# Optimization experiments

Hardware: AMD Instinct MI355X
Metric: run time of the kernel (lower is better)

The kernel has to match this reference:

```python
import jax, jax.numpy as jnp
import numpy as np

B, F, O = 32, 26, 20
IN, G = 2048, 512
REL = 53
EPS = 1e-5  # BatchNorm1d default eps


def setup_inputs() -> dict:
    key = jax.random.key(0)
    ks = jax.random.split(key, 10)
    inp = {
        "region_feats": jax.random.normal(ks[0], (B, F, O, IN), jnp.float32),
        "region_masks": jnp.ones((B, F, O), jnp.float32),
        "rel_feats": jax.random.randint(ks[1], (B, F, O, O), 0, REL, jnp.int64),
        "tem_feats": jax.random.uniform(ks[2], (B, F * O, F * O), jnp.float32),
        # learned params (eval mode: dropout off, BN uses running stats)
        "rel_W": jax.random.normal(ks[3], (G, IN), jnp.float32) * (1.0 / np.sqrt(IN)),
        "rel_b": jnp.zeros((G,), jnp.float32),
        "rel_emb": jax.random.normal(ks[4], (REL, G), jnp.float32) * 0.02,
        "tem_W": jax.random.normal(ks[5], (G, IN), jnp.float32) * (1.0 / np.sqrt(IN)),
        "tem_b": jnp.zeros((G,), jnp.float32),
        "bn_w": jnp.ones((F * O,), jnp.float32),
        "bn_b": jnp.zeros((F * O,), jnp.float32),
        "bn_rm": jnp.zeros((F * O,), jnp.float32),
        "bn_rv": jnp.ones((F * O,), jnp.float32),
    }
    return inp


def reference(region_feats, region_masks, rel_feats, tem_feats,
              rel_W, rel_b, rel_emb, tem_W, tem_b,
              bn_w, bn_b, bn_rm, bn_rv):
    b, f, o, _ = region_feats.shape
    # ---- RELATIONAL FEATURE GRAPH ----
    # [B,F,O,G]
    rel_region = jnp.einsum("bfoi,gi->bfog", region_feats, rel_W) + rel_b
    # embedding lookup: [B,F,O,O,G]
    emb = rel_emb[rel_feats]
    mask = (rel_feats > 0).astype(region_feats.dtype)  # [B,F,O,O]
    msum = jnp.sum(mask, axis=3)                        # [B,F,O]
    # sum_j mask_ij * emb_ij  (masked reduction over neighbor dim)
    emb_sum = jnp.einsum("bfijg,bfij->bfig", emb, mask)
    # sum_j mask_ij * r_i == r_i * msum_i, so (emb_sum + r*msum)/msum
    rel_out = (emb_sum + rel_region * msum[..., None]) / msum[..., None]
    rel_out = rel_out.reshape(b, f * o, -1)
    # ---- TEMPORAL FEATURE GRAPH ----
    tem_region = jnp.einsum("bfoi,gi->bfog", region_feats, tem_W) + tem_b
    tem_region = tem_region.reshape(b, f * o, -1)
    tem_sum = jnp.sum(tem_feats, axis=2)                # [B, F*O]
    tem_out = jnp.matmul(tem_feats, tem_region) / tem_sum[..., None]
    # ---- OUTPUT ----
    out = jnp.concatenate([rel_out, tem_out], axis=-1)  # [B, F*O, 2G]
    out = jnp.tanh(out)
    # BatchNorm1d over channel dim 1 (eval mode, running stats)
    inv = bn_w / jnp.sqrt(bn_rv + EPS)                  # [F*O]
    out = (out - bn_rm[None, :, None]) * inv[None, :, None] + bn_b[None, :, None]
    return out
```

## Files before the change

kernel.cpp:

```cpp
#include <hip/hip_runtime.h>
#include <stdint.h>

#define BB 32
#define FO 520
#define M1 16640
#define KIN 2048
#define KA 2112
#define N1 1024
#define GG 512
#define K2P 576
#define M2 640

typedef unsigned short u16;
typedef short v8s __attribute__((ext_vector_type(8)));
typedef float v4f __attribute__((ext_vector_type(4)));

__device__ __forceinline__ u16 f2bf(float f) {
  union { float f; unsigned u; } v; v.f = f;
  unsigned r = v.u + 0x7fffu + ((v.u >> 16) & 1u);
  return (u16)(r >> 16);
}

__device__ __forceinline__ float fast_tanh(float x) {
  float cx = fminf(fmaxf(x, -15.f), 15.f);
  float e = __expf(2.f * cx);
  return (e - 1.f) / (e + 1.f);
}

__global__ void prep_all_kernel(const float* __restrict__ rf, const int* __restrict__ rel,
                                const float* __restrict__ relW, const float* __restrict__ temW,
                                const float* __restrict__ emb, const float* __restrict__ tem,
                                u16* __restrict__ A1, u16* __restrict__ Wc,
                                u16* __restrict__ A2, float* __restrict__ tsum) {
  const int blk = blockIdx.x;
  const int t = threadIdx.x;
  if (blk < M1 + 1024) {
    const float* src;
    u16* orow;
    if (blk < M1) { src = rf + (size_t)blk * KIN; orow = A1 + (size_t)blk * KA; }
    else {
      const int n = blk - M1;
      src = (n < GG) ? (relW + (size_t)n * KIN) : (temW + (size_t)(n - GG) * KIN);
      orow = Wc + (size_t)n * KA;
    }
    const float4* p = (const float4*)src;
    float4 a = p[2 * t], b = p[2 * t + 1];
    v8s v;
    v[0] = (short)f2bf(a.x); v[1] = (short)f2bf(a.y);
    v[2] = (short)f2bf(a.z); v[3] = (short)f2bf(a.w);
    v[4] = (short)f2bf(b.x); v[5] = (short)f2bf(b.y);
    v[6] = (short)f2bf(b.z); v[7] = (short)f2bf(b.w);
    *(v8s*)(orow + t * 8) = v;
    if (t < 64) {
      float sval = 0.f;
      if (blk < M1) {
        const int* rp = rel + (size_t)blk * 20;
        int cnt = 0, ms = 0;
#pragma unroll
        for (int j = 0; j < 20; ++j) { int ix = rp[j]; cnt += (ix == t + 1); ms += (ix > 0); }
        if (t < 52 && ms > 0) sval = (float)cnt / (float)ms;
      } else {
        const int n = blk - M1;
        if (n < GG && t < 52) sval = emb[(size_t)(t + 1) * GG + n];
      }
      orow[KIN + t] = f2bf(sval);
    }
    return;
  }
  const int w = t >> 6, l = t & 63;
  const int row = (blk - (M1 + 1024)) * 4 + w;
  const int b = row / M2, i = row % M2;
  u16* orow = A2 + (size_t)row * K2P;
  v8s z = {0, 0, 0, 0, 0, 0, 0, 0};
  if (i >= FO) {
    *(v8s*)(orow + l * 8) = z;
    if (l < 8) *(v8s*)(orow + (64 + l) * 8) = z;
    return;
  }
  const float* srow = tem + ((size_t)b * FO + i) * FO;
  float s = 0.f;
  {
    float4 a = *(const float4*)(srow + 8 * l);
    float4 bb = *(const float4*)(srow + 8 * l + 4);
    s += a.x + a.y + a.z + a.w + bb.x + bb.y + bb.z + bb.w;
    v8s v;
    v[0] = (short)f2bf(a.x); v[1] = (short)f2bf(a.y);
    v[2] = (short)f2bf(a.z); v[3] = (short)f2bf(a.w);
    v[4] = (short)f2bf(bb.x); v[5] = (short)f2bf(bb.y);
    v[6] = (short)f2bf(bb.z); v[7] = (short)f2bf(bb.w);
    *(v8s*)(orow + l * 8) = v;
  }
  if (l < 8) {
    if (l == 0) {
      float4 a = *(const float4*)(srow + 512);
      float4 bb = *(const float4*)(srow + 516);
      s += a.x + a.y + a.z + a.w + bb.x + bb.y + bb.z + bb.w;
      v8s v;
      v[0] = (short)f2bf(a.x); v[1] = (short)f2bf(a.y);
      v[2] = (short)f2bf(a.z); v[3] = (short)f2bf(a.w);
      v[4] = (short)f2bf(bb.x); v[5] = (short)f2bf(bb.y);
      v[6] = (short)f2bf(bb.z); v[7] = (short)f2bf(bb.w);
      *(v8s*)(orow + 512) = v;
    } else {
      *(v8s*)(orow + (64 + l) * 8) = z;
    }
  }
#pragma unroll
  for (int off = 32; off > 0; off >>= 1) s += __shfl_down(s, off);
  if (l == 0) tsum[(size_t)b * FO + i] = s;
}


#define STAGE4(DST)                                                                              \
  do {                                                                                           \
    u16* dst_ = smem + (DST);                                                                    \
    __builtin_amdgcn_global_load_lds((const __attribute__((address_space(1))) void*)ga0,         \
        (__attribute__((address_space(3))) void*)(dst_ + lofA0), 16, 0, 0);                      \
    __builtin_amdgcn_global_load_lds((const __attribute__((address_space(1))) void*)gb0,         \
        (__attribute__((address_space(3))) void*)(dst_ + lofB0), 16, 0, 0);                      \
    __builtin_amdgcn_global_load_lds((const __attribute__((address_space(1))) void*)ga1,         \
        (__attribute__((address_space(3))) void*)(dst_ + lofA1), 16, 0, 0);                      \
    __builtin_amdgcn_global_load_lds((const __attribute__((address_space(1))) void*)gb1,         \
        (__attribute__((address_space(3))) void*)(dst_ + lofB1), 16, 0, 0);                      \
    ga0 += 32; gb0 += 32; ga1 += 32; gb1 += 32;                                                  \
  } while (0)

#define COMPUTE16(CB)                                                                            \
  do {                                                                                           \
    const u16* As_ = smem + (CB) * 8192;                                                         \
    const u16* Bs_ = As_ + 4096;                                                                 \
    v8s af[4], bf[4];                                                                            \
    _Pragma("unroll") for (int t4 = 0; t4 < 4; ++t4) {                                           \
      const int ra = wm * 64 + t4 * 16 + r16;                                                    \
      const int rb = wn * 64 + t4 * 16 + r16;                                                    \
      af[t4] = *(const v8s*)&As_[ra * 32 + ((quad ^ ((ra >> 1) & 3)) * 8)];                      \
      bf[t4] = *(const v8s*)&Bs_[rb * 32 + ((quad ^ ((rb >> 1) & 3)) * 8)];                      \
    }                                                                                            \
    _Pragma("unroll") for (int mtt = 0; mtt < 4; ++mtt)                                          \
      _Pragma("unroll") for (int ntt = 0; ntt < 4; ++ntt)                                        \
        acc[mtt][ntt] =                                                                          \
            __builtin_amdgcn_mfma_f32_16x16x32_bf16(af[mtt], bf[ntt], acc[mtt][ntt], 0, 0, 0);   \
  } while (0)

#define PIPE_TAIL(CB0, CB1)                                                                      \
  do {                                                                                           \
    asm volatile("s_waitcnt vmcnt(4)" ::: "memory");                                             \
    __builtin_amdgcn_s_barrier();                                                                \
    COMPUTE16(CB0);                                                                              \
    asm volatile("s_waitcnt lgkmcnt(0)" ::: "memory");                                           \
    __builtin_amdgcn_s_barrier();                                                                \
    asm volatile("s_waitcnt vmcnt(0)" ::: "memory");                                             \
    __builtin_amdgcn_s_barrier();                                                                \
    COMPUTE16(CB1);                                                                              \
  } while (0)

__global__ __launch_bounds__(256) void gemm1_kernel(
    const u16* __restrict__ A, const u16* __restrict__ Wc,
    const float* __restrict__ rel_b, const float* __restrict__ tem_b,
    const float* __restrict__ bn_w, const float* __restrict__ bn_b,
    const float* __restrict__ bn_rm, const float* __restrict__ bn_rv,
    float* __restrict__ out, u16* __restrict__ BT) {
  __shared__ u16 smem[24576];
  const int tid = threadIdx.x;
  const int lane = tid & 63;
  const int wv = tid >> 6, wm = wv >> 1, wn = wv & 1;
  const int id = blockIdx.x;
  const int x = id & 7, s = id >> 3;
  int mt, ntile;
  if (s < 128) { mt = x * 16 + (s >> 3); ntile = s & 7; }
  else         { mt = 128 + (s - 128);   ntile = x; }
  const int m0 = mt * 128, n0 = ntile * 128;
  const int quad = lane >> 4, r16 = lane & 15;

  const u16 *ga0, *ga1, *gb0, *gb1;
  {
    const int r0 = tid >> 2, sl0 = tid & 3;
    const int c0 = sl0 ^ ((r0 >> 1) & 3);
    ga0 = A + (size_t)(m0 + r0) * KA + c0 * 8;
    gb0 = Wc + (size_t)(n0 + r0) * KA + c0 * 8;
    const int L1 = 256 + tid;
    const int r1 = L1 >> 2, sl1 = L1 & 3;
    const int c1 = sl1 ^ ((r1 >> 1) & 3);
    ga1 = A + (size_t)(m0 + r1) * KA + c1 * 8;
    gb1 = Wc + (size_t)(n0 + r1) * KA + c1 * 8;
  }
  const int lofA0 = wv * 512, lofA1 = 2048 + wv * 512;
  const int lofB0 = 4096 + wv * 512, lofB1 = 6144 + wv * 512;

  v4f acc[4][4];
#pragma unroll
  for (int i = 0; i < 4; ++i)
#pragma unroll
    for (int j = 0; j < 4; ++j) { v4f z = {0.f, 0.f, 0.f, 0.f}; acc[i][j] = z; }

  STAGE4(0);
  STAGE4(8192);

  int cb = 0, nb = 2;
  for (int t = 0; t < 64; ++t) {
    STAGE4(nb * 8192);
    asm volatile("s_waitcnt vmcnt(8)" ::: "memory");
    __builtin_amdgcn_s_barrier();
    COMPUTE16(cb);
    asm volatile("s_waitcnt lgkmcnt(0)" ::: "memory");
    __builtin_amdgcn_s_barrier();
    cb = (cb == 2) ? 0 : cb + 1;
    nb = (nb == 2) ? 0 : nb + 1;
  }
  PIPE_TAIL(cb, (cb == 2) ? 0 : cb + 1);

  if (n0 < GG) {
#pragma unroll
    for (int mtt = 0; mtt < 4; ++mtt) {
      const int mb = m0 + wm * 64 + mtt * 16 + quad * 4;
      const int bb = mb / FO;
      const int fo0 = mb - bb * FO;
      float inv[4], rm[4], bofs[4];
#pragma unroll
      for (int r = 0; r < 4; ++r) {
        const int fo = fo0 + r;
        inv[r] = bn_w[fo] * rsqrtf(bn_rv[fo] + 1e-5f);
        rm[r] = bn_rm[fo]; bofs[r] = bn_b[fo];
      }
#pragma unroll
      for (int ntt = 0; ntt < 4; ++ntt) {
        const int n = n0 + wn * 64 + ntt * 16 + r16;
        const float rbn = rel_b[n];
#pragma unroll
        for (int r = 0; r < 4; ++r) {
          float val = (fast_tanh(acc[mtt][ntt][r] + rbn) - rm[r]) * inv[r] + bofs[r];
          __builtin_nontemporal_store(val, out + (size_t)(mb + r) * N1 + n);
        }
      }
    }
  } else {
    __syncthreads();
#pragma unroll
    for (int p = 0; p < 2; ++p) {
      if (p) __syncthreads();
      if (wn == p) {
#pragma unroll
        for (int mtt = 0; mtt < 4; ++mtt) {
          const int il = wm * 64 + mtt * 16 + quad * 4;
#pragma unroll
          for (int ntt = 0; ntt < 4; ++ntt) {
            const int gl = ntt * 16 + r16;
            const float tb = tem_b[(n0 - GG) + p * 64 + gl];
            ushort4 w;
            w.x = f2bf(acc[mtt][ntt][0] + tb);
            w.y = f2bf(acc[mtt][ntt][1] + tb);
            w.z = f2bf(acc[mtt][ntt][2] + tb);
            w.w = f2bf(acc[mtt][ntt][3] + tb);
            *(ushort4*)&smem[gl * 136 + il] = w;
          }
        }
      }
      __syncthreads();
#pragma unroll
      for (int pass = 0; pass < 4; ++pass) {
        const int gl = pass * 16 + (tid >> 4);
        const int ch = tid & 15;
        const int m = m0 + ch * 8;
        const int b1 = m / FO;
        const int i1 = m - b1 * FO;
        v8s val = *(const v8s*)&smem[gl * 136 + ch * 8];
        const int g = (n0 - GG) + p * 64 + gl;
        *(v8s*)(BT + ((size_t)(b1 * GG + g)) * K2P + i1) = val;
      }
    }
  }
}

__global__ __launch_bounds__(256) void gemm2_kernel(
    const u16* __restrict__ A2, const u16* __restrict__ BT,
    const float* __restrict__ tsum,
    const float* __restrict__ bn_w, const float* __restrict__ bn_b,
    const float* __restrict__ bn_rm, const float* __restrict__ bn_rv,
    float* __restrict__ out) {
  __shared__ u16 smem[24576];
  const int tid = threadIdx.x;
  const int lane = tid & 63;
  const int wv = tid >> 6, wm = wv >> 1, wn = wv & 1;
  const int m0 = blockIdx.x * 128;
  const int n0 = blockIdx.y * 128;
  const int b = blockIdx.z;
  const u16* Ab = A2 + (size_t)b * M2 * K2P;
  const u16* Bb = BT + (size_t)b * GG * K2P;
  const int quad = lane >> 4, r16 = lane & 15;

  const u16 *ga0, *ga1, *gb0, *gb1;
  {
    const int r0 = tid >> 2, sl0 = tid & 3;
    const int c0 = sl0 ^ ((r0 >> 1) & 3);
    ga0 = Ab + (size_t)(m0 + r0) * K2P + c0 * 8;
    gb0 = Bb + (size_t)(n0 + r0) * K2P + c0 * 8;
    const int L1 = 256 + tid;
    const int r1 = L1 >> 2, sl1 = L1 & 3;
    const int c1 = sl1 ^ ((r1 >> 1) & 3);
    ga1 = Ab + (size_t)(m0 + r1) * K2P + c1 * 8;
    gb1 = Bb + (size_t)(n0 + r1) * K2P + c1 * 8;
  }
  const int lofA0 = wv * 512, lofA1 = 2048 + wv * 512;
  const int lofB0 = 4096 + wv * 512, lofB1 = 6144 + wv * 512;

  v4f acc[4][4];
#pragma unroll
  for (int i = 0; i < 4; ++i)
#pragma unroll
    for (int j = 0; j < 4; ++j) { v4f z = {0.f, 0.f, 0.f, 0.f}; acc[i][j] = z; }

  STAGE4(0);
  STAGE4(8192);

  int cb = 0, nb = 2;
  for (int t = 0; t < 16; ++t) {
    STAGE4(nb * 8192);
    asm volatile("s_waitcnt vmcnt(8)" ::: "memory");
    __builtin_amdgcn_s_barrier();
    COMPUTE16(cb);
    asm volatile("s_waitcnt lgkmcnt(0)" ::: "memory");
    __builtin_amdgcn_s_barrier();
    cb = (cb == 2) ? 0 : cb + 1;
    nb = (nb == 2) ? 0 : nb + 1;
  }
  PIPE_TAIL(cb, (cb == 2) ? 0 : cb + 1);

#pragma unroll
  for (int mtt = 0; mtt < 4; ++mtt) {
    const int ibase = m0 + wm * 64 + mtt * 16 + quad * 4;
    if (ibase >= FO) continue;
    float ts[4], inv[4], rm[4], bofs[4];
#pragma unroll
    for (int r = 0; r < 4; ++r) {
      const int i = ibase + r;
      ts[r] = 1.f / tsum[(size_t)b * FO + i];
      inv[r] = bn_w[i] * rsqrtf(bn_rv[i] + 1e-5f);
      rm[r] = bn_rm[i]; bofs[r] = bn_b[i];
    }
#pragma unroll
    for (int ntt = 0; ntt < 4; ++ntt) {
      const int g = n0 + wn * 64 + ntt * 16 + r16;
#pragma unroll
      for (int r = 0; r < 4; ++r) {
        float val = (fast_tanh(acc[mtt][ntt][r] * ts[r]) - rm[r]) * inv[r] + bofs[r];
        __builtin_nontemporal_store(val, out + ((size_t)(b * FO + (ibase + r))) * N1 + GG + g);
      }
    }
  }
}

extern "C" void kernel_launch(void* const* d_in, const int* in_sizes, int n_in,
                              void* d_out, int out_size, void* d_ws, size_t ws_size,
                              hipStream_t stream) {
  const float* region_feats = (const float*)d_in[0];
  const int* rel_feats = (const int*)d_in[2];
  const float* tem_feats = (const float*)d_in[3];
  const float* rel_W = (const float*)d_in[4];
  const float* rel_b = (const float*)d_in[5];
  const float* rel_emb = (const float*)d_in[6];
  const float* tem_W = (const float*)d_in[7];
  const float* tem_b = (const float*)d_in[8];
  const float* bn_w = (const float*)d_in[9];
  const float* bn_b = (const float*)d_in[10];
  const float* bn_rm = (const float*)d_in[11];
  const float* bn_rv = (const float*)d_in[12];
  float* out = (float*)d_out;

  char* base = (char*)d_ws;
  u16* A1 = (u16*)base;
  u16* Wc = (u16*)(base + 70287360);
  u16* A2 = (u16*)(base + 74612736);
  u16* BT = (u16*)(base + 98205696);
  float* tsum = (float*)(base + 117080064);

  prep_all_kernel<<<M1 + 1024 + 5120, 256, 0, stream>>>(
      region_feats, rel_feats, rel_W, tem_W, rel_emb, tem_feats, A1, Wc, A2, tsum);
  gemm1_kernel<<<1040, 256, 0, stream>>>(A1, Wc, rel_b, tem_b,
                                         bn_w, bn_b, bn_rm, bn_rv, out, BT);
  gemm2_kernel<<<dim3(5, 4, 32), 256, 0, stream>>>(A2, BT, tsum,
                                                   bn_w, bn_b, bn_rm, bn_rv, out);
}
```

Before: 406.6 us.

## Enlarge gemm1 block tile to 256x128 with 512 threads and new block mapping

gemm1 now uses 512-thread blocks (8 waves) that compute a 256x128 output tile, halving the grid to 520 blocks and sharing each staged B tile across twice as many rows. The block-to-tile mapping is replaced with a simpler interleaved scheme, LDS grows to 72 KB for a three-stage buffer, and the epilogue transpose for the temporal half is widened accordingly. The pipeline tail in both GEMMs is simplified by merging a barrier. The aim is to cut global/L2 traffic for the weight operand and raise MFMA reuse, at the cost of more LDS per block and possibly lower occupancy.

Result: no change. 399.6 us (-1.7%).

```diff
diff --git a/kernel.cpp b/kernel.cpp
--- a/kernel.cpp
+++ b/kernel.cpp
@@ -110,8 +110,156 @@
   if (l == 0) tsum[(size_t)b * FO + i] = s;
 }
 
-
-#define STAGE4(DST)                                                                              \
+#define G1_STAGE(DST)                                                                            \
+  do {                                                                                           \
+    u16* dst_ = smem + (DST);                                                                    \
+    __builtin_amdgcn_global_load_lds((const __attribute__((address_space(1))) void*)ga0,         \
+        (__attribute__((address_space(3))) void*)(dst_ + lofA0), 16, 0, 0);                      \
+    __builtin_amdgcn_global_load_lds((const __attribute__((address_space(1))) void*)ga1,         \
+        (__attribute__((address_space(3))) void*)(dst_ + lofA1), 16, 0, 0);                      \
+    __builtin_amdgcn_global_load_lds((const __attribute__((address_space(1))) void*)gb0,         \
+        (__attribute__((address_space(3))) void*)(dst_ + lofB0), 16, 0, 0);                      \
+    ga0 += 32; ga1 += 32; gb0 += 32;                                                             \
+  } while (0)
+
+#define G1_COMPUTE(CB)                                                                           \
+  do {                                                                                           \
+    const u16* As_ = smem + (CB) * 12288;                                                        \
+    const u16* Bs_ = As_ + 8192;                                                                 \
+    v8s af[4], bf[4];                                                                            \
+    _Pragma("unroll") for (int t4 = 0; t4 < 4; ++t4) {                                           \
+      const int ra = wm * 64 + t4 * 16 + r16;                                                    \
+      const int rb = wn * 64 + t4 * 16 + r16;                                                    \
+      af[t4] = *(const v8s*)&As_[ra * 32 + ((quad ^ ((ra >> 1) & 3)) * 8)];                      \
+      bf[t4] = *(const v8s*)&Bs_[rb * 32 + ((quad ^ ((rb >> 1) & 3)) * 8)];                      \
+    }                                                                                            \
+    _Pragma("unroll") for (int mtt = 0; mtt < 4; ++mtt)                                          \
+      _Pragma("unroll") for (int ntt = 0; ntt < 4; ++ntt)                                        \
+        acc[mtt][ntt] =                                                                          \
+            __builtin_amdgcn_mfma_f32_16x16x32_bf16(af[mtt], bf[ntt], acc[mtt][ntt], 0, 0, 0);   \
+  } while (0)
+
+__global__ __launch_bounds__(512, 4) void gemm1_kernel(
+    const u16* __restrict__ A, const u16* __restrict__ Wc,
+    const float* __restrict__ rel_b, const float* __restrict__ tem_b,
+    const float* __restrict__ bn_w, const float* __restrict__ bn_b,
+    const float* __restrict__ bn_rm, const float* __restrict__ bn_rv,
+    float* __restrict__ out, u16* __restrict__ BT) {
+  __shared__ u16 smem[36864];
+  const int tid = threadIdx.x;
+  const int lane = tid & 63;
+  const int wv = tid >> 6, wm = wv >> 1, wn = wv & 1;
+  const int id = blockIdx.x;
+  const int wgid = (id & 7) * 65 + (id >> 3);
+  const int mt = wgid >> 3, nt = wgid & 7;
+  const int m0 = mt * 256, n0 = nt * 128;
+  const int quad = lane >> 4, r16 = lane & 15;
+
+  const u16 *ga0, *ga1, *gb0;
+  {
+    const int r0 = tid >> 2, sl0 = tid & 3;
+    ga0 = A + (size_t)(m0 + r0) * KA + (sl0 ^ ((r0 >> 1) & 3)) * 8;
+    const int r1 = 128 + (tid >> 2);
+    ga1 = A + (size_t)(m0 + r1) * KA + (sl0 ^ ((r1 >> 1) & 3)) * 8;
+    gb0 = Wc + (size_t)(n0 + r0) * KA + (sl0 ^ ((r0 >> 1) & 3)) * 8;
+  }
+  const int lofA0 = wv * 512;
+  const int lofA1 = 4096 + wv * 512;
+  const int lofB0 = 8192 + wv * 512;
+
+  v4f acc[4][4];
+#pragma unroll
+  for (int i = 0; i < 4; ++i)
+#pragma unroll
+    for (int j = 0; j < 4; ++j) { v4f z = {0.f, 0.f, 0.f, 0.f}; acc[i][j] = z; }
+
+  G1_STAGE(0);
+  G1_STAGE(12288);
+
+  int cb = 0, nb = 2;
+  for (int t = 0; t < 64; ++t) {
+    G1_STAGE(nb * 12288);
+    asm volatile("s_waitcnt vmcnt(6)" ::: "memory");
+    __builtin_amdgcn_s_barrier();
+    G1_COMPUTE(cb);
+    asm volatile("s_waitcnt lgkmcnt(0)" ::: "memory");
+    __builtin_amdgcn_s_barrier();
+    cb = (cb == 2) ? 0 : cb + 1;
+    nb = (nb == 2) ? 0 : nb + 1;
+  }
+  {
+    const int cb1 = (cb == 2) ? 0 : cb + 1;
+    asm volatile("s_waitcnt vmcnt(3)" ::: "memory");
+    __builtin_amdgcn_s_barrier();
+    G1_COMPUTE(cb);
+    asm volatile("s_waitcnt vmcnt(0) lgkmcnt(0)" ::: "memory");
+    __builtin_amdgcn_s_barrier();
+    G1_COMPUTE(cb1);
+  }
+
+  if (n0 < GG) {
+#pragma unroll
+    for (int mtt = 0; mtt < 4; ++mtt) {
+      const int mb = m0 + wm * 64 + mtt * 16 + quad * 4;
+      const int bb = mb / FO;
+      const int fo0 = mb - bb * FO;
+      float inv[4], rm[4], bofs[4];
+#pragma unroll
+      for (int r = 0; r < 4; ++r) {
+        const int fo = fo0 + r;
+        inv[r] = bn_w[fo] * rsqrtf(bn_rv[fo] + 1e-5f);
+        rm[r] = bn_rm[fo]; bofs[r] = bn_b[fo];
+      }
+#pragma unroll
+      for (int ntt = 0; ntt < 4; ++ntt) {
+        const int n = n0 + wn * 64 + ntt * 16 + r16;
+        const float rbn = rel_b[n];
+#pragma unroll
+        for (int r = 0; r < 4; ++r) {
+          float val = (fast_tanh(acc[mtt][ntt][r] + rbn) - rm[r]) * inv[r] + bofs[r];
+          __builtin_nontemporal_store(val, out + (size_t)(mb + r) * N1 + n);
+        }
+      }
+    }
+  } else {
+    __syncthreads();
+#pragma unroll
+    for (int p = 0; p < 2; ++p) {
+      if (p) __syncthreads();
+      if (wn == p) {
+#pragma unroll
+        for (int mtt = 0; mtt < 4; ++mtt) {
+          const int il = wm * 64 + mtt * 16 + quad * 4;
+#pragma unroll
+          for (int ntt = 0; ntt < 4; ++ntt) {
+            const int gl = ntt * 16 + r16;
+            const float tb = tem_b[(n0 - GG) + p * 64 + gl];
+            ushort4 w;
+            w.x = f2bf(acc[mtt][ntt][0] + tb);
+            w.y = f2bf(acc[mtt][ntt][1] + tb);
+            w.z = f2bf(acc[mtt][ntt][2] + tb);
+            w.w = f2bf(acc[mtt][ntt][3] + tb);
+            *(ushort4*)&smem[gl * 264 + il] = w;
+          }
+        }
+      }
+      __syncthreads();
+#pragma unroll
+      for (int pass = 0; pass < 4; ++pass) {
+        const int gl = pass * 16 + (tid >> 5);
+        const int ch = tid & 31;
+        const int m = m0 + ch * 8;
+        const int b1 = m / FO;
+        const int i1 = m - b1 * FO;
+        v8s val = *(const v8s*)&smem[gl * 264 + ch * 8];
+        const int g = (n0 - GG) + p * 64 + gl;
+        *(v8s*)(BT + ((size_t)(b1 * GG + g)) * K2P + i1) = val;
+      }
+    }
+  }
+}
+
+#define G2_STAGE(DST)                                                                            \
   do {                                                                                           \
     u16* dst_ = smem + (DST);                                                                    \
     __builtin_amdgcn_global_load_lds((const __attribute__((address_space(1))) void*)ga0,         \
@@ -125,7 +273,7 @@
     ga0 += 32; gb0 += 32; ga1 += 32; gb1 += 32;                                                  \
   } while (0)
 
-#define COMPUTE16(CB)                                                                            \
+#define G2_COMPUTE(CB)                                                                           \
   do {                                                                                           \
     const u16* As_ = smem + (CB) * 8192;                                                         \
     const u16* Bs_ = As_ + 4096;                                                                 \
@@ -141,135 +289,6 @@
         acc[mtt][ntt] =                                                                          \
             __builtin_amdgcn_mfma_f32_16x16x32_bf16(af[mtt], bf[ntt], acc[mtt][ntt], 0, 0, 0);   \
   } while (0)
-
-#define PIPE_TAIL(CB0, CB1)                                                                      \
-  do {                                                                                           \
-    asm volatile("s_waitcnt vmcnt(4)" ::: "memory");                                             \
-    __builtin_amdgcn_s_barrier();                                                                \
-    COMPUTE16(CB0);                                                                              \
-    asm volatile("s_waitcnt lgkmcnt(0)" ::: "memory");                                           \
-    __builtin_amdgcn_s_barrier();                                                                \
-    asm volatile("s_waitcnt vmcnt(0)" ::: "memory");                                             \
-    __builtin_amdgcn_s_barrier();                                                                \
-    COMPUTE16(CB1);                                                                              \
-  } while (0)
-
-__global__ __launch_bounds__(256) void gemm1_kernel(
-    const u16* __restrict__ A, const u16* __restrict__ Wc,
-    const float* __restrict__ rel_b, const float* __restrict__ tem_b,
-    const float* __restrict__ bn_w, const float* __restrict__ bn_b,
-    const float* __restrict__ bn_rm, const float* __restrict__ bn_rv,
-    float* __restrict__ out, u16* __restrict__ BT) {
-  __shared__ u16 smem[24576];
-  const int tid = threadIdx.x;
-  const int lane = tid & 63;
-  const int wv = tid >> 6, wm = wv >> 1, wn = wv & 1;
-  const int id = blockIdx.x;
-  const int x = id & 7, s = id >> 3;
-  int mt, ntile;
-  if (s < 128) { mt = x * 16 + (s >> 3); ntile = s & 7; }
-  else         { mt = 128 + (s - 128);   ntile = x; }
-  const int m0 = mt * 128, n0 = ntile * 128;
-  const int quad = lane >> 4, r16 = lane & 15;
-
-  const u16 *ga0, *ga1, *gb0, *gb1;
-  {
-    const int r0 = tid >> 2, sl0 = tid & 3;
-    const int c0 = sl0 ^ ((r0 >> 1) & 3);
-    ga0 = A + (size_t)(m0 + r0) * KA + c0 * 8;
-    gb0 = Wc + (size_t)(n0 + r0) * KA + c0 * 8;
-    const int L1 = 256 + tid;
-    const int r1 = L1 >> 2, sl1 = L1 & 3;
-    const int c1 = sl1 ^ ((r1 >> 1) & 3);
-    ga1 = A + (size_t)(m0 + r1) * KA + c1 * 8;
-    gb1 = Wc + (size_t)(n0 + r1) * KA + c1 * 8;
-  }
-  const int lofA0 = wv * 512, lofA1 = 2048 + wv * 512;
-  const int lofB0 = 4096 + wv * 512, lofB1 = 6144 + wv * 512;
-
-  v4f acc[4][4];
-#pragma unroll
-  for (int i = 0; i < 4; ++i)
-#pragma unroll
-    for (int j = 0; j < 4; ++j) { v4f z = {0.f, 0.f, 0.f, 0.f}; acc[i][j] = z; }
-
-  STAGE4(0);
-  STAGE4(8192);
-
-  int cb = 0, nb = 2;
-  for (int t = 0; t < 64; ++t) {
-    STAGE4(nb * 8192);
-    asm volatile("s_waitcnt vmcnt(8)" ::: "memory");
-    __builtin_amdgcn_s_barrier();
-    COMPUTE16(cb);
-    asm volatile("s_waitcnt lgkmcnt(0)" ::: "memory");
-    __builtin_amdgcn_s_barrier();
-    cb = (cb == 2) ? 0 : cb + 1;
-    nb = (nb == 2) ? 0 : nb + 1;
-  }
-  PIPE_TAIL(cb, (cb == 2) ? 0 : cb + 1);
-
-  if (n0 < GG) {
-#pragma unroll
-    for (int mtt = 0; mtt < 4; ++mtt) {
-      const int mb = m0 + wm * 64 + mtt * 16 + quad * 4;
-      const int bb = mb / FO;
-      const int fo0 = mb - bb * FO;
-      float inv[4], rm[4], bofs[4];
-#pragma unroll
-      for (int r = 0; r < 4; ++r) {
-        const int fo = fo0 + r;
-        inv[r] = bn_w[fo] * rsqrtf(bn_rv[fo] + 1e-5f);
-        rm[r] = bn_rm[fo]; bofs[r] = bn_b[fo];
-      }
-#pragma unroll
-      for (int ntt = 0; ntt < 4; ++ntt) {
-        const int n = n0 + wn * 64 + ntt * 16 + r16;
-        const float rbn = rel_b[n];
-#pragma unroll
-        for (int r = 0; r < 4; ++r) {
-          float val = (fast_tanh(acc[mtt][ntt][r] + rbn) - rm[r]) * inv[r] + bofs[r];
-          __builtin_nontemporal_store(val, out + (size_t)(mb + r) * N1 + n);
-        }
-      }
-    }
-  } else {
-    __syncthreads();
-#pragma unroll
-    for (int p = 0; p < 2; ++p) {
-      if (p) __syncthreads();
-      if (wn == p) {
-#pragma unroll
-        for (int mtt = 0; mtt < 4; ++mtt) {
-          const int il = wm * 64 + mtt * 16 + quad * 4;
-#pragma unroll
-          for (int ntt = 0; ntt < 4; ++ntt) {
-            const int gl = ntt * 16 + r16;
-            const float tb = tem_b[(n0 - GG) + p * 64 + gl];
-            ushort4 w;
-            w.x = f2bf(acc[mtt][ntt][0] + tb);
-            w.y = f2bf(acc[mtt][ntt][1] + tb);
-            w.z = f2bf(acc[mtt][ntt][2] + tb);
-            w.w = f2bf(acc[mtt][ntt][3] + tb);
-            *(ushort4*)&smem[gl * 136 + il] = w;
-          }
-        }
-      }
-      __syncthreads();
-#pragma unroll
-      for (int pass = 0; pass < 4; ++pass) {
-        const int gl = pass * 16 + (tid >> 4);
-        const int ch = tid & 15;
-        const int m = m0 + ch * 8;
-        const int b1 = m / FO;
-        const int i1 = m - b1 * FO;
-        v8s val = *(const v8s*)&smem[gl * 136 + ch * 8];
-        const int g = (n0 - GG) + p * 64 + gl;
-        *(v8s*)(BT + ((size_t)(b1 * GG + g)) * K2P + i1) = val;
-      }
-    }
-  }
-}
 
 __global__ __launch_bounds__(256) void gemm2_kernel(
     const u16* __restrict__ A2, const u16* __restrict__ BT,
@@ -309,21 +328,29 @@
 #pragma unroll
     for (int j = 0; j < 4; ++j) { v4f z = {0.f, 0.f, 0.f, 0.f}; acc[i][j] = z; }
 
-  STAGE4(0);
-  STAGE4(8192);
+  G2_STAGE(0);
+  G2_STAGE(8192);
 
   int cb = 0, nb = 2;
   for (int t = 0; t < 16; ++t) {
-    STAGE4(nb * 8192);
+    G2_STAGE(nb * 8192);
     asm volatile("s_waitcnt vmcnt(8)" ::: "memory");
     __builtin_amdgcn_s_barrier();
-    COMPUTE16(cb);
+    G2_COMPUTE(cb);
     asm volatile("s_waitcnt lgkmcnt(0)" ::: "memory");
     __builtin_amdgcn_s_barrier();
     cb = (cb == 2) ? 0 : cb + 1;
     nb = (nb == 2) ? 0 : nb + 1;
   }
-  PIPE_TAIL(cb, (cb == 2) ? 0 : cb + 1);
+  {
+    const int cb1 = (cb == 2) ? 0 : cb + 1;
+    asm volatile("s_waitcnt vmcnt(4)" ::: "memory");
+    __builtin_amdgcn_s_barrier();
+    G2_COMPUTE(cb);
+    asm volatile("s_waitcnt vmcnt(0) lgkmcnt(0)" ::: "memory");
+    __builtin_amdgcn_s_barrier();
+    G2_COMPUTE(cb1);
+  }
 
 #pragma unroll
   for (int mtt = 0; mtt < 4; ++mtt) {
@@ -375,8 +402,8 @@
 
   prep_all_kernel<<<M1 + 1024 + 5120, 256, 0, stream>>>(
       region_feats, rel_feats, rel_W, tem_W, rel_emb, tem_feats, A1, Wc, A2, tsum);
-  gemm1_kernel<<<1040, 256, 0, stream>>>(A1, Wc, rel_b, tem_b,
-                                         bn_w, bn_b, bn_rm, bn_rv, out, BT);
+  gemm1_kernel<<<520, 512, 0, stream>>>(A1, Wc, rel_b, tem_b,
+                                        bn_w, bn_b, bn_rm, bn_rv, out, BT);
   gemm2_kernel<<<dim3(5, 4, 32), 256, 0, stream>>>(A2, BT, tsum,
                                                    bn_w, bn_b, bn_rm, bn_rv, out);
 }
```
